# Kernel tuning notes

Hardware: AMD Instinct MI355X
Metric: run time of the kernel (lower is better)

The kernel has to match this reference:

```python
import jax, jax.numpy as jnp
import numpy as np

HIDDEN = 1024
NUM_HEADS = 16
HOP_NUM = 1023  # seq_len = hop_num + 1 = 1024
ATT_SIZE = HIDDEN // NUM_HEADS
SCALE = ATT_SIZE ** (-0.5)
B, S = 8, HOP_NUM + 1


def setup_inputs() -> dict:
    key = jax.random.key(0)
    ks = jax.random.split(key, 13)
    lim = 1.0 / np.sqrt(HIDDEN)
    return {
        "q": jax.random.normal(ks[0], (B, S, HIDDEN), jnp.float32),
        "k": jax.random.normal(ks[1], (B, S, HIDDEN), jnp.float32),
        "v": jax.random.normal(ks[2], (B, S, HIDDEN), jnp.float32),
        "attn_bias": jax.random.normal(ks[3], (B, 1, S, S), jnp.float32),
        "Wq": jax.random.uniform(ks[4], (HIDDEN, HIDDEN), jnp.float32, -lim, lim),
        "bq": jax.random.uniform(ks[5], (HIDDEN,), jnp.float32, -lim, lim),
        "Wk": jax.random.uniform(ks[6], (HIDDEN, HIDDEN), jnp.float32, -lim, lim),
        "bk": jax.random.uniform(ks[7], (HIDDEN,), jnp.float32, -lim, lim),
        "Wv": jax.random.uniform(ks[8], (HIDDEN, HIDDEN), jnp.float32, -lim, lim),
        "bv": jax.random.uniform(ks[9], (HIDDEN,), jnp.float32, -lim, lim),
        "Wo": jax.random.uniform(ks[10], (HIDDEN, HIDDEN), jnp.float32, -lim, lim),
        "bo": jax.random.uniform(ks[11], (HIDDEN,), jnp.float32, -lim, lim),
        "zoom_bias": jax.random.normal(ks[12], (2 * HOP_NUM + 1, 1), jnp.float32),
    }


def reference(q, k, v, attn_bias, Wq, bq, Wk, bk, Wv, bv, Wo, bo, zoom_bias):
    b, s, _ = q.shape
    # projections -> [b, s, h, d]
    qh = (q @ Wq.T + bq).reshape(b, s, NUM_HEADS, ATT_SIZE)
    kh = (k @ Wk.T + bk).reshape(b, s, NUM_HEADS, ATT_SIZE)
    vh = (v @ Wv.T + bv).reshape(b, s, NUM_HEADS, ATT_SIZE)
    # relative zoom encoding: ze[i, j] = zoom_bias[i - j + hop_num]
    idx = jnp.arange(s)[:, None] - jnp.arange(s)[None, :] + HOP_NUM
    ze = zoom_bias[idx, 0]  # [s, s]
    # scaled dot-product attention with additive zoom bias
    scores = jnp.einsum("bshd,bthd->bhst", qh * SCALE, kh) + ze + attn_bias
    probs = jax.nn.softmax(scores, axis=-1)
    out = jnp.einsum("bhst,bthd->bshd", probs, vh).reshape(b, s, NUM_HEADS * ATT_SIZE)
    return out @ Wo.T + bo
```

## Files before the change

### kernel.cpp

```cpp
#include <hip/hip_runtime.h>
#include <cstdint>


#define SQ   1024
#define HID  1024
#define CEXP 0.18033688f
#define LOG2E 1.44269504f

typedef __attribute__((ext_vector_type(8))) __bf16 bf16x8;
typedef __attribute__((ext_vector_type(8))) unsigned short ushort8;
typedef __attribute__((ext_vector_type(4))) float  floatx4;

__device__ __forceinline__ float b2f(unsigned short x) {
    return __builtin_bit_cast(float, (uint32_t)x << 16);
}
__device__ __forceinline__ unsigned short f2bf(float f) {
    uint32_t u = __builtin_bit_cast(uint32_t, f);
    u += 0x7fffu + ((u >> 16) & 1u);
    return (unsigned short)(u >> 16);
}

__device__ __forceinline__ void glds16(const void* g, void* l) {
    __builtin_amdgcn_global_load_lds(
        (const __attribute__((address_space(1))) void*)g,
        (__attribute__((address_space(3))) void*)l, 16, 0, 0);
}

__global__ void cvt(const float* __restrict__ s, unsigned short* __restrict__ d,
                    int n4, float scale) {
    const int i = blockIdx.x * blockDim.x + threadIdx.x;
    if (i >= n4) return;
    const floatx4 v = *(const floatx4*)(s + 4 * (size_t)i);
    uint32_t lo = (uint32_t)f2bf(v[0] * scale) | ((uint32_t)f2bf(v[1] * scale) << 16);
    uint32_t hi = (uint32_t)f2bf(v[2] * scale) | ((uint32_t)f2bf(v[3] * scale) << 16);
    ((uint2*)d)[i] = make_uint2(lo, hi);
}

__global__ void cvt3(const float* __restrict__ s0, const float* __restrict__ s1,
                     const float* __restrict__ s2, unsigned short* __restrict__ d0,
                     unsigned short* __restrict__ d1, unsigned short* __restrict__ d2,
                     int n4) {
    const int i = blockIdx.x * blockDim.x + threadIdx.x;
    if (i >= n4) return;
    const int z = blockIdx.y;
    const float* s = z == 0 ? s0 : (z == 1 ? s1 : s2);
    unsigned short* d = z == 0 ? d0 : (z == 1 ? d1 : d2);
    const floatx4 v = *(const floatx4*)(s + 4 * (size_t)i);
    uint32_t lo = (uint32_t)f2bf(v[0]) | ((uint32_t)f2bf(v[1]) << 16);
    uint32_t hi = (uint32_t)f2bf(v[2]) | ((uint32_t)f2bf(v[3]) << 16);
    ((uint2*)d)[i] = make_uint2(lo, hi);
}

__global__ void cvt4(const float* __restrict__ s0, const float* __restrict__ s1,
                     const float* __restrict__ s2, const float* __restrict__ s3,
                     unsigned short* __restrict__ d0, unsigned short* __restrict__ d1,
                     unsigned short* __restrict__ d2, unsigned short* __restrict__ d3,
                     int n4) {
    const int i = blockIdx.x * blockDim.x + threadIdx.x;
    if (i >= n4) return;
    const int z = blockIdx.y;
    const float* s = z == 0 ? s0 : (z == 1 ? s1 : (z == 2 ? s2 : s3));
    unsigned short* d = z == 0 ? d0 : (z == 1 ? d1 : (z == 2 ? d2 : d3));
    const floatx4 v = *(const floatx4*)(s + 4 * (size_t)i);
    uint32_t lo = (uint32_t)f2bf(v[0]) | ((uint32_t)f2bf(v[1]) << 16);
    uint32_t hi = (uint32_t)f2bf(v[2]) | ((uint32_t)f2bf(v[3]) << 16);
    ((uint2*)d)[i] = make_uint2(lo, hi);
}

__global__ __launch_bounds__(256) void gemm_qkv(
    const short* __restrict__ Aq, const short* __restrict__ Ak,
    const short* __restrict__ Av, const short* __restrict__ Wq_,
    const short* __restrict__ Wk_, const short* __restrict__ Wv_,
    const float* __restrict__ bq_, const float* __restrict__ bk_,
    const float* __restrict__ bv_, short* __restrict__ oq,
    short* __restrict__ ok, short* __restrict__ ov)
{
    __shared__ __align__(16) short As[4096];
    __shared__ __align__(16) short Bs[4096];

    const int z = blockIdx.z;
    const short* A    = z == 0 ? Aq  : (z == 1 ? Ak  : Av);
    const short* Bw   = z == 0 ? Wq_ : (z == 1 ? Wk_ : Wv_);
    const float* bias = z == 0 ? bq_ : (z == 1 ? bk_ : bv_);
    short* C          = z == 0 ? oq  : (z == 1 ? ok  : ov);
    const bool trans  = (z == 2);

    const int tid = threadIdx.x;
    const int w = tid >> 6, lane = tid & 63;
    const int quad = lane >> 4, c = lane & 15;
    const int wr = w >> 1, wc = w & 1;

    const int nwg = gridDim.x * gridDim.y;
    const int id  = blockIdx.y * gridDim.x + blockIdx.x;
    const int nid = (id & 7) * (nwg >> 3) + (id >> 3);
    const int bn = nid & 7, bm = nid >> 3;

    const short* ag0 = A  + (size_t)(bm * 128 + w * 16 + c) * HID + quad * 8;
    const short* ag1 = ag0 + (size_t)64 * HID;
    const short* bg0 = Bw + (size_t)(bn * 128 + w * 16 + c) * HID + quad * 8;
    const short* bg1 = bg0 + (size_t)64 * HID;

    floatx4 acc[4][4] = {};

    for (int kt = 0; kt < 32; ++kt) {
        __syncthreads();
        glds16(ag0, As + w * 512);
        glds16(ag1, As + (w + 4) * 512);
        glds16(bg0, Bs + w * 512);
        glds16(bg1, Bs + (w + 4) * 512);
        asm volatile("s_waitcnt vmcnt(0)" ::: "memory");
        __syncthreads();
        ag0 += 32; ag1 += 32; bg0 += 32; bg1 += 32;

        bf16x8 a[4], b[4];
#pragma unroll
        for (int i = 0; i < 4; ++i)
            a[i] = *(const bf16x8*)(As + (wr * 4 + i) * 512 + lane * 8);
#pragma unroll
        for (int j = 0; j < 4; ++j)
            b[j] = *(const bf16x8*)(Bs + (wc * 4 + j) * 512 + lane * 8);
#pragma unroll
        for (int i = 0; i < 4; ++i)
#pragma unroll
            for (int j = 0; j < 4; ++j)
                acc[i][j] = __builtin_amdgcn_mfma_f32_16x16x32_bf16(a[i], b[j], acc[i][j], 0, 0, 0);
    }

    float bsv[4];
#pragma unroll
    for (int j = 0; j < 4; ++j)
        bsv[j] = bias[bn * 128 + wc * 64 + j * 16 + c];

#pragma unroll
    for (int i = 0; i < 4; ++i) {
#pragma unroll
        for (int j = 0; j < 4; ++j) {
            const int n = bn * 128 + wc * 64 + j * 16 + c;
#pragma unroll
            for (int r = 0; r < 4; ++r) {
                const int row = bm * 128 + wr * 64 + i * 16 + quad * 4 + r;
                const float val = acc[i][j][r] + bsv[j];
                const size_t idx = trans
                    ? ((size_t)(row >> 10) * HID + n) * SQ + (row & 1023)
                    : (size_t)row * HID + n;
                C[idx] = (short)f2bf(val);
            }
        }
    }
}

__global__ __launch_bounds__(256) void gemm_bt(
    const short* __restrict__ A, const short* __restrict__ Bw,
    const float* __restrict__ bias, float* __restrict__ C, size_t cOff)
{
    __shared__ __align__(16) short As[4096];
    __shared__ __align__(16) short Bs[4096];

    const int tid = threadIdx.x;
    const int w = tid >> 6, lane = tid & 63;
    const int quad = lane >> 4, c = lane & 15;
    const int wr = w >> 1, wc = w & 1;

    const int nwg = gridDim.x * gridDim.y;
    const int id  = blockIdx.y * gridDim.x + blockIdx.x;
    const int nid = (id & 7) * (nwg >> 3) + (id >> 3);
    const int bn = nid & 7, bm = nid >> 3;

    const short* ag0 = A  + (size_t)(bm * 128 + w * 16 + c) * HID + quad * 8;
    const short* ag1 = ag0 + (size_t)64 * HID;
    const short* bg0 = Bw + (size_t)(bn * 128 + w * 16 + c) * HID + quad * 8;
    const short* bg1 = bg0 + (size_t)64 * HID;

    floatx4 acc[4][4] = {};

    for (int kt = 0; kt < 32; ++kt) {
        __syncthreads();
        glds16(ag0, As + w * 512);
        glds16(ag1, As + (w + 4) * 512);
        glds16(bg0, Bs + w * 512);
        glds16(bg1, Bs + (w + 4) * 512);
        asm volatile("s_waitcnt vmcnt(0)" ::: "memory");
        __syncthreads();
        ag0 += 32; ag1 += 32; bg0 += 32; bg1 += 32;

        bf16x8 a[4], b[4];
#pragma unroll
        for (int i = 0; i < 4; ++i)
            a[i] = *(const bf16x8*)(As + (wr * 4 + i) * 512 + lane * 8);
#pragma unroll
        for (int j = 0; j < 4; ++j)
            b[j] = *(const bf16x8*)(Bs + (wc * 4 + j) * 512 + lane * 8);
#pragma unroll
        for (int i = 0; i < 4; ++i)
#pragma unroll
            for (int j = 0; j < 4; ++j)
                acc[i][j] = __builtin_amdgcn_mfma_f32_16x16x32_bf16(a[i], b[j], acc[i][j], 0, 0, 0);
    }

    float bsv[4];
#pragma unroll
    for (int j = 0; j < 4; ++j)
        bsv[j] = bias[bn * 128 + wc * 64 + j * 16 + c];

#pragma unroll
    for (int i = 0; i < 4; ++i)
#pragma unroll
        for (int j = 0; j < 4; ++j) {
            const int n = bn * 128 + wc * 64 + j * 16 + c;
#pragma unroll
            for (int r = 0; r < 4; ++r) {
                const int row = bm * 128 + wr * 64 + i * 16 + quad * 4 + r;
                C[cOff + (size_t)row * HID + n] = acc[i][j][r] + bsv[j];
            }
        }
}

__global__ __launch_bounds__(256) void attn(
    const short* __restrict__ qh, const short* __restrict__ kh,
    const short* __restrict__ vht, const unsigned short* __restrict__ abc,
    const float* __restrict__ zbf, short* __restrict__ aout, int b0)
{
    __shared__ __align__(16) short Kf[4096];
    __shared__ __align__(16) short Vf[4096];
    __shared__ __align__(16) short Ps[4][2304];
    __shared__ float Zs[1152];

    const int tid = threadIdx.x;
    const int w = tid >> 6, lane = tid & 63;
    const int quad = lane >> 4, c = lane & 15;

    int qb, h, bl;
    if (gridDim.z == 8) {
        const int B = blockIdx.x + (blockIdx.y << 3) + (blockIdx.z << 7);
        const int hb = (B >> 6) * 8 + (B & 7);
        qb = (B >> 3) & 7; h = hb & 15; bl = hb >> 4;
    } else {
        qb = blockIdx.x; h = blockIdx.y; bl = blockIdx.z;
    }
    const int b = b0 + bl;

    for (int j = tid; j < 1151; j += 256)
        Zs[j] = zbf[qb * 128 + j] * LOG2E;

    const size_t blS = (size_t)bl * SQ;

    bf16x8 qa[2][2];
#pragma unroll
    for (int m = 0; m < 2; ++m)
#pragma unroll
        for (int half = 0; half < 2; ++half)
            qa[m][half] = *(const bf16x8*)(qh + (blS + qb * 128 + w * 32 + m * 16 + c) * HID
                                               + h * 64 + half * 32 + quad * 8);

    const short* kg = kh  + (blS + 2 * c + (w & 1)) * HID + h * 64 + (w >> 1) * 32 + quad * 8;
    const short* vg = vht + ((size_t)bl * HID + h * 64 + w * 16 + c) * SQ + quad * 8;
    const size_t bge = ((size_t)b * SQ + qb * 128 + w * 32 + quad * 4) * SQ;

    bf16x8 kv0 = *(const bf16x8*)kg, kv1 = *(const bf16x8*)(kg + 32 * HID);
    bf16x8 vv0 = *(const bf16x8*)vg, vv1 = *(const bf16x8*)(vg + 32);

    uint32_t bp[2][4][2];
    auto loadB = [&](int K0) {
#pragma unroll
        for (int m = 0; m < 2; ++m)
#pragma unroll
            for (int r = 0; r < 4; ++r)
#pragma unroll
                for (int sub = 0; sub < 2; ++sub)
                    bp[m][r][sub] = *(const uint32_t*)(abc + bge + (size_t)(m * 16 + r) * SQ
                                                        + K0 + sub * 32 + 2 * c);
    };
    loadB(0);

    floatx4 o[2][4] = {};
    float sume[2][4] = {};

    for (int kt = 0; kt < 16; ++kt) {
        __syncthreads();
        *(bf16x8*)(Kf + w * 512 + lane * 8)       = kv0;
        *(bf16x8*)(Kf + (w + 4) * 512 + lane * 8) = kv1;
        *(bf16x8*)(Vf + w * 512 + lane * 8)       = vv0;
        *(bf16x8*)(Vf + (w + 4) * 512 + lane * 8) = vv1;
        __syncthreads();

        if (kt < 15) {
            kg += 64 * HID; vg += 64;
            kv0 = *(const bf16x8*)kg; kv1 = *(const bf16x8*)(kg + 32 * HID);
            vv0 = *(const bf16x8*)vg; vv1 = *(const bf16x8*)(vg + 32);
        }

        floatx4 sc[2][2][2] = {};
        __builtin_amdgcn_s_setprio(1);
#pragma unroll
        for (int sub = 0; sub < 2; ++sub) {
            bf16x8 kf[2][2];
#pragma unroll
            for (int half = 0; half < 2; ++half)
#pragma unroll
                for (int kb = 0; kb < 2; ++kb)
                    kf[half][kb] = *(const bf16x8*)(Kf + (sub * 4 + half * 2 + kb) * 512 + lane * 8);
#pragma unroll
            for (int m = 0; m < 2; ++m)
#pragma unroll
                for (int kb = 0; kb < 2; ++kb) {
                    sc[m][sub][kb] = __builtin_amdgcn_mfma_f32_16x16x32_bf16(qa[m][0], kf[0][kb], sc[m][sub][kb], 0, 0, 0);
                    sc[m][sub][kb] = __builtin_amdgcn_mfma_f32_16x16x32_bf16(qa[m][1], kf[1][kb], sc[m][sub][kb], 0, 0, 0);
                }
        }
        __builtin_amdgcn_s_setprio(0);

        const int k0 = kt * 64;
#pragma unroll
        for (int m = 0; m < 2; ++m) {
#pragma unroll
            for (int r = 0; r < 4; ++r) {
                const int lrq = w * 32 + m * 16 + quad * 4 + r;
                const int tb = lrq + 1023 - k0;
#pragma unroll
                for (int sub = 0; sub < 2; ++sub) {
                    const int kl = sub * 32 + 2 * c;
                    const uint32_t bv_ = bp[m][r][sub];
                    const float z0 = Zs[tb - kl], z1 = Zs[tb - kl - 1];
                    const float s0 = sc[m][sub][0][r] * CEXP + z0 + b2f((unsigned short)(bv_ & 0xffffu));
                    const float s1 = sc[m][sub][1][r] * CEXP + z1
                                   + __builtin_bit_cast(float, bv_ & 0xffff0000u);
                    const float e0 = __builtin_amdgcn_exp2f(s0);
                    const float e1 = __builtin_amdgcn_exp2f(s1);
                    sume[m][r] += e0 + e1;
                    const uint32_t pp = (uint32_t)f2bf(e0) | ((uint32_t)f2bf(e1) << 16);
                    *(uint32_t*)(&Ps[w][0] + (m * 16 + quad * 4 + r) * 72 + kl) = pp;
                }
            }
        }

        if (kt < 15) loadB(k0 + 64);

        __builtin_amdgcn_s_setprio(1);
#pragma unroll
        for (int sub = 0; sub < 2; ++sub) {
            bf16x8 ap[2];
#pragma unroll
            for (int m = 0; m < 2; ++m)
                ap[m] = *(const bf16x8*)(&Ps[w][0] + (m * 16 + c) * 72 + sub * 32 + quad * 8);
#pragma unroll
            for (int dt = 0; dt < 4; ++dt) {
                const bf16x8 vf = *(const bf16x8*)(Vf + (sub * 4 + dt) * 512 + lane * 8);
#pragma unroll
                for (int m = 0; m < 2; ++m)
                    o[m][dt] = __builtin_amdgcn_mfma_f32_16x16x32_bf16(ap[m], vf, o[m][dt], 0, 0, 0);
            }
        }
        __builtin_amdgcn_s_setprio(0);
    }

#pragma unroll
    for (int m = 0; m < 2; ++m)
#pragma unroll
        for (int r = 0; r < 4; ++r) {
            float s = sume[m][r];
            s += __shfl_xor(s, 1);
            s += __shfl_xor(s, 2);
            s += __shfl_xor(s, 4);
            s += __shfl_xor(s, 8);
            sume[m][r] = 1.0f / s;
        }

#pragma unroll
    for (int m = 0; m < 2; ++m)
#pragma unroll
        for (int dt = 0; dt < 4; ++dt)
#pragma unroll
            for (int r = 0; r < 4; ++r) {
                const size_t row = blS + qb * 128 + w * 32 + m * 16 + quad * 4 + r;
                ((unsigned short*)aout)[row * HID + h * 64 + dt * 16 + c] =
                    f2bf(o[m][dt][r] * sume[m][r]);
            }
}

extern "C" void kernel_launch(void* const* d_in, const int* in_sizes, int n_in,
                              void* d_out, int out_size, void* d_ws, size_t ws_size,
                              hipStream_t stream) {
    const float* q  = (const float*)d_in[0];
    const float* k  = (const float*)d_in[1];
    const float* v  = (const float*)d_in[2];
    const float* ab = (const float*)d_in[3];
    const float* Wq = (const float*)d_in[4];  const float* bq = (const float*)d_in[5];
    const float* Wk = (const float*)d_in[6];  const float* bk = (const float*)d_in[7];
    const float* Wv = (const float*)d_in[8];  const float* bv = (const float*)d_in[9];
    const float* Wo = (const float*)d_in[10]; const float* bo = (const float*)d_in[11];
    const float* zb = (const float*)d_in[12];

    const size_t perB = (size_t)SQ * HID;
    const size_t WN   = (size_t)HID * HID;

    int G = 8;
    while (G > 1 && 24ull * 1024 * 1024 + 12ull * G * perB > ws_size) G >>= 1;

    unsigned short* Wqc = (unsigned short*)d_ws;
    unsigned short* Wkc = Wqc + WN;
    unsigned short* Wvc = Wkc + WN;
    unsigned short* Woc = Wvc + WN;
    unsigned short* abc = Woc + WN;
    short* cbq = (short*)(abc + 8 * perB);
    short* cbk = cbq + (size_t)G * perB;
    short* cbv = cbk + (size_t)G * perB;
    short* qh  = cbv + (size_t)G * perB;
    short* khp = qh  + (size_t)G * perB;
    short* vht = khp + (size_t)G * perB;
    short* ao  = cbq;

    const dim3 bt(256);
    const int ngroups = 8 / G;
    const int cn4 = (int)(G * perB / 4);
    const int cgrid = (cn4 + 255) / 256;

    cvt4<<<dim3((WN / 4 + 255) / 256, 4), 256, 0, stream>>>(
        Wq, Wk, Wv, Wo, Wqc, Wkc, Wvc, Woc, (int)(WN / 4));
    cvt<<<(8 * perB / 4 + 255) / 256, 256, 0, stream>>>(ab, abc, 8 * perB / 4, LOG2E);

    for (int g = 0; g < ngroups; ++g) {
        const size_t off = (size_t)g * G * perB;
        cvt3<<<dim3(cgrid, 3), 256, 0, stream>>>(
            q + off, k + off, v + off,
            (unsigned short*)cbq, (unsigned short*)cbk, (unsigned short*)cbv, cn4);
        gemm_qkv<<<dim3(8, G * 8, 3), bt, 0, stream>>>(
            cbq, cbk, cbv, (short*)Wqc, (short*)Wkc, (short*)Wvc,
            bq, bk, bv, qh, khp, vht);
        attn<<<dim3(8, 16, G), bt, 0, stream>>>(qh, khp, vht, abc, zb, ao, g * G);
        gemm_bt<<<dim3(8, G * 8), bt, 0, stream>>>(ao, (short*)Woc, bo, (float*)d_out, off);
    }
}
```

Baseline: 415.0 us.

## Rewrite projection GEMMs with 256x256 tiles, double-buffered LDS and interleaved prefetch

Both GEMM kernels now share one core that computes 256x256 output tiles with 512 threads, a K step of 64, and double-buffered LDS. Global-to-LDS loads for the next K step are interleaved with the MFMA groups of the current step, and the MFMA groups run at raised wave priority. This targets the per-iteration load/wait/barrier stalls and the low data reuse of the older 128x128 single-buffered loop. The cost is 128KB of LDS per block and many more accumulators per thread, which limits occupancy and leaves fewer blocks to fill the CUs.

```diff
diff --git a/kernel.cpp b/kernel.cpp
--- a/kernel.cpp
+++ b/kernel.cpp
@@ -8,7 +8,6 @@
 #define LOG2E 1.44269504f
 
 typedef __attribute__((ext_vector_type(8))) __bf16 bf16x8;
-typedef __attribute__((ext_vector_type(8))) unsigned short ushort8;
 typedef __attribute__((ext_vector_type(4))) float  floatx4;
 
 __device__ __forceinline__ float b2f(unsigned short x) {
@@ -67,7 +66,142 @@
     ((uint2*)d)[i] = make_uint2(lo, hi);
 }
 
-__global__ __launch_bounds__(256) void gemm_qkv(
+__device__ __forceinline__ void gemm256_core(
+    const short* __restrict__ A, const short* __restrict__ Bw,
+    const float* __restrict__ bias, void* __restrict__ C, size_t cOff,
+    int bm, int bn, bool trans, bool outF32,
+    short (*As2)[16384], short (*Bs2)[16384])
+{
+    const int tid = threadIdx.x;
+    const int wid = tid >> 6, lane = tid & 63;
+    const int quad = lane >> 4, cc = lane & 15;
+    const int wr = wid >> 2, wc = wid & 3;
+
+    const int skh = wid >> 2;
+    const int sr0 = (wid & 3) * 4;
+    const size_t AU = (size_t)16 * HID;
+
+    const short* ag = A  + (size_t)(bm * 256 + sr0 * 16 + cc) * HID + skh * 32 + quad * 8;
+    const short* bg = Bw + (size_t)(bn * 256 + sr0 * 16 + cc) * HID + skh * 32 + quad * 8;
+    const int dA = skh * 8192 + sr0 * 512;
+    const int dB = dA;
+
+    floatx4 acc[8][4] = {};
+
+#pragma unroll
+    for (int u = 0; u < 4; ++u) glds16(ag + u * AU, As2[0] + dA + u * 512);
+#pragma unroll
+    for (int u = 0; u < 4; ++u) glds16(bg + u * AU, Bs2[0] + dB + u * 512);
+    ag += 64; bg += 64;
+
+    for (int kt = 0; kt < 16; ++kt) {
+        const int b = kt & 1;
+        asm volatile("s_waitcnt vmcnt(0)" ::: "memory");
+        __builtin_amdgcn_s_barrier();
+        __builtin_amdgcn_sched_barrier(0);
+        const bool st = (kt < 15);
+        short* Ad = As2[b ^ 1];
+        short* Bd = Bs2[b ^ 1];
+        const short* Ab = As2[b];
+        const short* Bb = Bs2[b];
+
+        bf16x8 aF[4][2], bF0[2][2], bF1[2][2];
+
+        if (st) { glds16(ag + 0 * AU, Ad + dA + 0 * 512);
+                  glds16(ag + 1 * AU, Ad + dA + 1 * 512); }
+#pragma unroll
+        for (int i = 0; i < 4; ++i)
+#pragma unroll
+            for (int kh = 0; kh < 2; ++kh)
+                aF[i][kh] = *(const bf16x8*)(Ab + kh * 8192 + (wr * 8 + i) * 512 + lane * 8);
+#pragma unroll
+        for (int j = 0; j < 2; ++j)
+#pragma unroll
+            for (int kh = 0; kh < 2; ++kh)
+                bF0[j][kh] = *(const bf16x8*)(Bb + kh * 8192 + (wc * 4 + j) * 512 + lane * 8);
+        __builtin_amdgcn_s_setprio(1);
+#pragma unroll
+        for (int i = 0; i < 4; ++i)
+#pragma unroll
+            for (int j = 0; j < 2; ++j)
+#pragma unroll
+                for (int kh = 0; kh < 2; ++kh)
+                    acc[i][j] = __builtin_amdgcn_mfma_f32_16x16x32_bf16(aF[i][kh], bF0[j][kh], acc[i][j], 0, 0, 0);
+        __builtin_amdgcn_s_setprio(0);
+
+        if (st) { glds16(ag + 2 * AU, Ad + dA + 2 * 512);
+                  glds16(ag + 3 * AU, Ad + dA + 3 * 512); }
+#pragma unroll
+        for (int j = 0; j < 2; ++j)
+#pragma unroll
+            for (int kh = 0; kh < 2; ++kh)
+                bF1[j][kh] = *(const bf16x8*)(Bb + kh * 8192 + (wc * 4 + 2 + j) * 512 + lane * 8);
+        __builtin_amdgcn_s_setprio(1);
+#pragma unroll
+        for (int i = 0; i < 4; ++i)
+#pragma unroll
+            for (int j = 0; j < 2; ++j)
+#pragma unroll
+                for (int kh = 0; kh < 2; ++kh)
+                    acc[i][2 + j] = __builtin_amdgcn_mfma_f32_16x16x32_bf16(aF[i][kh], bF1[j][kh], acc[i][2 + j], 0, 0, 0);
+        __builtin_amdgcn_s_setprio(0);
+
+        if (st) { glds16(bg + 0 * AU, Bd + dB + 0 * 512);
+                  glds16(bg + 1 * AU, Bd + dB + 1 * 512); }
+#pragma unroll
+        for (int i = 0; i < 4; ++i)
+#pragma unroll
+            for (int kh = 0; kh < 2; ++kh)
+                aF[i][kh] = *(const bf16x8*)(Ab + kh * 8192 + (wr * 8 + 4 + i) * 512 + lane * 8);
+        __builtin_amdgcn_s_setprio(1);
+#pragma unroll
+        for (int i = 0; i < 4; ++i)
+#pragma unroll
+            for (int j = 0; j < 2; ++j)
+#pragma unroll
+                for (int kh = 0; kh < 2; ++kh)
+                    acc[4 + i][j] = __builtin_amdgcn_mfma_f32_16x16x32_bf16(aF[i][kh], bF0[j][kh], acc[4 + i][j], 0, 0, 0);
+        __builtin_amdgcn_s_setprio(0);
+
+        if (st) { glds16(bg + 2 * AU, Bd + dB + 2 * 512);
+                  glds16(bg + 3 * AU, Bd + dB + 3 * 512);
+                  ag += 64; bg += 64; }
+        __builtin_amdgcn_s_setprio(1);
+#pragma unroll
+        for (int i = 0; i < 4; ++i)
+#pragma unroll
+            for (int j = 0; j < 2; ++j)
+#pragma unroll
+                for (int kh = 0; kh < 2; ++kh)
+                    acc[4 + i][2 + j] = __builtin_amdgcn_mfma_f32_16x16x32_bf16(aF[i][kh], bF1[j][kh], acc[4 + i][2 + j], 0, 0, 0);
+        __builtin_amdgcn_s_setprio(0);
+    }
+
+    float bsv[4];
+#pragma unroll
+    for (int j = 0; j < 4; ++j)
+        bsv[j] = bias[bn * 256 + wc * 64 + j * 16 + cc];
+
+#pragma unroll
+    for (int i = 0; i < 8; ++i) {
+#pragma unroll
+        for (int j = 0; j < 4; ++j) {
+            const int n = bn * 256 + wc * 64 + j * 16 + cc;
+#pragma unroll
+            for (int r = 0; r < 4; ++r) {
+                const int row = bm * 256 + wr * 128 + i * 16 + quad * 4 + r;
+                const float val = acc[i][j][r] + bsv[j];
+                size_t idx;
+                if (trans) idx = ((size_t)(row >> 10) * HID + n) * SQ + (row & 1023);
+                else       idx = (size_t)row * HID + n;
+                if (outF32) ((float*)C)[cOff + idx] = val;
+                else        ((unsigned short*)C)[cOff + idx] = f2bf(val);
+            }
+        }
+    }
+}
+
+__global__ __launch_bounds__(512) void gemm_qkv(
     const short* __restrict__ Aq, const short* __restrict__ Ak,
     const short* __restrict__ Av, const short* __restrict__ Wq_,
     const short* __restrict__ Wk_, const short* __restrict__ Wv_,
@@ -75,144 +209,36 @@
     const float* __restrict__ bv_, short* __restrict__ oq,
     short* __restrict__ ok, short* __restrict__ ov)
 {
-    __shared__ __align__(16) short As[4096];
-    __shared__ __align__(16) short Bs[4096];
+    __shared__ __align__(16) short As2[2][16384];
+    __shared__ __align__(16) short Bs2[2][16384];
 
     const int z = blockIdx.z;
     const short* A    = z == 0 ? Aq  : (z == 1 ? Ak  : Av);
     const short* Bw   = z == 0 ? Wq_ : (z == 1 ? Wk_ : Wv_);
     const float* bias = z == 0 ? bq_ : (z == 1 ? bk_ : bv_);
     short* C          = z == 0 ? oq  : (z == 1 ? ok  : ov);
-    const bool trans  = (z == 2);
-
-    const int tid = threadIdx.x;
-    const int w = tid >> 6, lane = tid & 63;
-    const int quad = lane >> 4, c = lane & 15;
-    const int wr = w >> 1, wc = w & 1;
 
     const int nwg = gridDim.x * gridDim.y;
     const int id  = blockIdx.y * gridDim.x + blockIdx.x;
     const int nid = (id & 7) * (nwg >> 3) + (id >> 3);
-    const int bn = nid & 7, bm = nid >> 3;
-
-    const short* ag0 = A  + (size_t)(bm * 128 + w * 16 + c) * HID + quad * 8;
-    const short* ag1 = ag0 + (size_t)64 * HID;
-    const short* bg0 = Bw + (size_t)(bn * 128 + w * 16 + c) * HID + quad * 8;
-    const short* bg1 = bg0 + (size_t)64 * HID;
-
-    floatx4 acc[4][4] = {};
-
-    for (int kt = 0; kt < 32; ++kt) {
-        __syncthreads();
-        glds16(ag0, As + w * 512);
-        glds16(ag1, As + (w + 4) * 512);
-        glds16(bg0, Bs + w * 512);
-        glds16(bg1, Bs + (w + 4) * 512);
-        asm volatile("s_waitcnt vmcnt(0)" ::: "memory");
-        __syncthreads();
-        ag0 += 32; ag1 += 32; bg0 += 32; bg1 += 32;
-
-        bf16x8 a[4], b[4];
-#pragma unroll
-        for (int i = 0; i < 4; ++i)
-            a[i] = *(const bf16x8*)(As + (wr * 4 + i) * 512 + lane * 8);
-#pragma unroll
-        for (int j = 0; j < 4; ++j)
-            b[j] = *(const bf16x8*)(Bs + (wc * 4 + j) * 512 + lane * 8);
-#pragma unroll
-        for (int i = 0; i < 4; ++i)
-#pragma unroll
-            for (int j = 0; j < 4; ++j)
-                acc[i][j] = __builtin_amdgcn_mfma_f32_16x16x32_bf16(a[i], b[j], acc[i][j], 0, 0, 0);
-    }
-
-    float bsv[4];
-#pragma unroll
-    for (int j = 0; j < 4; ++j)
-        bsv[j] = bias[bn * 128 + wc * 64 + j * 16 + c];
-
-#pragma unroll
-    for (int i = 0; i < 4; ++i) {
-#pragma unroll
-        for (int j = 0; j < 4; ++j) {
-            const int n = bn * 128 + wc * 64 + j * 16 + c;
-#pragma unroll
-            for (int r = 0; r < 4; ++r) {
-                const int row = bm * 128 + wr * 64 + i * 16 + quad * 4 + r;
-                const float val = acc[i][j][r] + bsv[j];
-                const size_t idx = trans
-                    ? ((size_t)(row >> 10) * HID + n) * SQ + (row & 1023)
-                    : (size_t)row * HID + n;
-                C[idx] = (short)f2bf(val);
-            }
-        }
-    }
-}
-
-__global__ __launch_bounds__(256) void gemm_bt(
+    const int bn = nid & 3, bm = nid >> 2;
+
+    gemm256_core(A, Bw, bias, C, 0, bm, bn, z == 2, false, As2, Bs2);
+}
+
+__global__ __launch_bounds__(512) void gemm_bt(
     const short* __restrict__ A, const short* __restrict__ Bw,
     const float* __restrict__ bias, float* __restrict__ C, size_t cOff)
 {
-    __shared__ __align__(16) short As[4096];
-    __shared__ __align__(16) short Bs[4096];
-
-    const int tid = threadIdx.x;
-    const int w = tid >> 6, lane = tid & 63;
-    const int quad = lane >> 4, c = lane & 15;
-    const int wr = w >> 1, wc = w & 1;
+    __shared__ __align__(16) short As2[2][16384];
+    __shared__ __align__(16) short Bs2[2][16384];
 
     const int nwg = gridDim.x * gridDim.y;
     const int id  = blockIdx.y * gridDim.x + blockIdx.x;
     const int nid = (id & 7) * (nwg >> 3) + (id >> 3);
-    const int bn = nid & 7, bm = nid >> 3;
-
-    const short* ag0 = A  + (size_t)(bm * 128 + w * 16 + c) * HID + quad * 8;
-    const short* ag1 = ag0 + (size_t)64 * HID;
-    const short* bg0 = Bw + (size_t)(bn * 128 + w * 16 + c) * HID + quad * 8;
-    const short* bg1 = bg0 + (size_t)64 * HID;
-
-    floatx4 acc[4][4] = {};
-
-    for (int kt = 0; kt < 32; ++kt) {
-        __syncthreads();
-        glds16(ag0, As + w * 512);
-        glds16(ag1, As + (w + 4) * 512);
-        glds16(bg0, Bs + w * 512);
-        glds16(bg1, Bs + (w + 4) * 512);
-        asm volatile("s_waitcnt vmcnt(0)" ::: "memory");
-        __syncthreads();
-        ag0 += 32; ag1 += 32; bg0 += 32; bg1 += 32;
-
-        bf16x8 a[4], b[4];
-#pragma unroll
-        for (int i = 0; i < 4; ++i)
-            a[i] = *(const bf16x8*)(As + (wr * 4 + i) * 512 + lane * 8);
-#pragma unroll
-        for (int j = 0; j < 4; ++j)
-            b[j] = *(const bf16x8*)(Bs + (wc * 4 + j) * 512 + lane * 8);
-#pragma unroll
-        for (int i = 0; i < 4; ++i)
-#pragma unroll
-            for (int j = 0; j < 4; ++j)
-                acc[i][j] = __builtin_amdgcn_mfma_f32_16x16x32_bf16(a[i], b[j], acc[i][j], 0, 0, 0);
-    }
-
-    float bsv[4];
-#pragma unroll
-    for (int j = 0; j < 4; ++j)
-        bsv[j] = bias[bn * 128 + wc * 64 + j * 16 + c];
-
-#pragma unroll
-    for (int i = 0; i < 4; ++i)
-#pragma unroll
-        for (int j = 0; j < 4; ++j) {
-            const int n = bn * 128 + wc * 64 + j * 16 + c;
-#pragma unroll
-            for (int r = 0; r < 4; ++r) {
-                const int row = bm * 128 + wr * 64 + i * 16 + quad * 4 + r;
-                C[cOff + (size_t)row * HID + n] = acc[i][j][r] + bsv[j];
-            }
-        }
+    const int bn = nid & 3, bm = nid >> 2;
+
+    gemm256_core(A, Bw, bias, C, cOff, bm, bn, false, true, As2, Bs2);
 }
 
 __global__ __launch_bounds__(256) void attn(
@@ -409,10 +435,10 @@
     short* vht = khp + (size_t)G * perB;
     short* ao  = cbq;
 
-    const dim3 bt(256);
     const int ngroups = 8 / G;
     const int cn4 = (int)(G * perB / 4);
     const int cgrid = (cn4 + 255) / 256;
+    const int mb = G * 4;
 
     cvt4<<<dim3((WN / 4 + 255) / 256, 4), 256, 0, stream>>>(
         Wq, Wk, Wv, Wo, Wqc, Wkc, Wvc, Woc, (int)(WN / 4));
@@ -423,10 +449,10 @@
         cvt3<<<dim3(cgrid, 3), 256, 0, stream>>>(
             q + off, k + off, v + off,
             (unsigned short*)cbq, (unsigned short*)cbk, (unsigned short*)cbv, cn4);
-        gemm_qkv<<<dim3(8, G * 8, 3), bt, 0, stream>>>(
+        gemm_qkv<<<dim3(4, mb, 3), dim3(512), 0, stream>>>(
             cbq, cbk, cbv, (short*)Wqc, (short*)Wkc, (short*)Wvc,
             bq, bk, bv, qh, khp, vht);
-        attn<<<dim3(8, 16, G), bt, 0, stream>>>(qh, khp, vht, abc, zb, ao, g * G);
-        gemm_bt<<<dim3(8, G * 8), bt, 0, stream>>>(ao, (short*)Woc, bo, (float*)d_out, off);
+        attn<<<dim3(8, 16, G), dim3(256), 0, stream>>>(qh, khp, vht, abc, zb, ao, g * G);
+        gemm_bt<<<dim3(4, mb), dim3(512), 0, stream>>>(ao, (short*)Woc, bo, (float*)d_out, off);
     }
 }
```

Result: no change. 422.3 us (+1.7%).
